# Kernel tuning notes

Hardware: AMD Instinct MI355X
Metric: run time of the kernel (lower is better)

Reference implementation:

```python
import jax, jax.numpy as jnp
from jax import lax
import numpy as np

B, T, F, H, L = 64, 2048, 8, 128, 2


def _uniform(key, shape, k):
    return jax.random.uniform(key, shape, jnp.float32, -k, k)


def setup_inputs() -> dict:
    key = jax.random.key(0)
    keys = jax.random.split(key, 12)
    k = 1.0 / np.sqrt(H)
    inp = {"x": jax.random.normal(keys[0], (B, T, F), jnp.float32)}
    # layer 0: input size F; layer 1: input size H (PyTorch nn.LSTM layout: gates i,f,g,o)
    inp["w_ih0"] = _uniform(keys[1], (4 * H, F), k)
    inp["w_hh0"] = _uniform(keys[2], (4 * H, H), k)
    inp["b_ih0"] = _uniform(keys[3], (4 * H,), k)
    inp["b_hh0"] = _uniform(keys[4], (4 * H,), k)
    inp["w_ih1"] = _uniform(keys[5], (4 * H, H), k)
    inp["w_hh1"] = _uniform(keys[6], (4 * H, H), k)
    inp["b_ih1"] = _uniform(keys[7], (4 * H,), k)
    inp["b_hh1"] = _uniform(keys[8], (4 * H,), k)
    inp["w_lin"] = _uniform(keys[9], (F, H), 1.0 / np.sqrt(H))
    inp["b_lin"] = _uniform(keys[10], (F,), 1.0 / np.sqrt(H))
    return inp


def _lstm_layer(x, w_ih, w_hh, b_ih, b_hh):
    # x: [B, T, D_in]; precompute input contribution to gates: [B, T, 4H]
    xg = jnp.einsum('btd,gd->btg', x, w_ih) + b_ih + b_hh
    h0 = jnp.zeros((x.shape[0], w_hh.shape[1]), x.dtype)
    c0 = jnp.zeros_like(h0)

    def step(carry, xg_t):
        h, c = carry
        gates = xg_t + h @ w_hh.T  # [B, 4H]
        i, f, g, o = jnp.split(gates, 4, axis=-1)
        i = jax.nn.sigmoid(i)
        f = jax.nn.sigmoid(f)
        g = jnp.tanh(g)
        o = jax.nn.sigmoid(o)
        c = f * c + i * g
        h = o * jnp.tanh(c)
        return (h, c), h

    _, hs = lax.scan(step, (h0, c0), jnp.swapaxes(xg, 0, 1))  # hs: [T, B, H]
    return jnp.swapaxes(hs, 0, 1)


def reference(x, w_ih0, w_hh0, b_ih0, b_hh0, w_ih1, w_hh1, b_ih1, b_hh1, w_lin, b_lin):
    h = _lstm_layer(x, w_ih0, w_hh0, b_ih0, b_hh0)
    h = _lstm_layer(h, w_ih1, w_hh1, b_ih1, b_hh1)
    return jnp.einsum('bth,fh->btf', h, w_lin) + b_lin
```

## Files before the change

kernel.cpp:

```cpp
#include <hip/hip_runtime.h>

#define B_ 64
#define T_ 2048
#define F_ 8
#define H_ 128
#define RING_LD 68
#define CHUNK 64
#define NCH (T_ / CHUNK)
#define GRING 16
#define H0_DW (CHUNK * 64)

typedef _Float16 v2h   __attribute__((ext_vector_type(2)));
typedef _Float16 f16x8 __attribute__((ext_vector_type(8)));
typedef float    f32x4 __attribute__((ext_vector_type(4)));

__device__ __forceinline__ unsigned pk2h(float lo, float hi) {
    v2h p;
    p[0] = (_Float16)lo;
    p[1] = (_Float16)hi;
    return __builtin_bit_cast(unsigned, p);
}

#if __has_builtin(__builtin_amdgcn_fdot2)
__device__ __forceinline__ float fdot2a(unsigned a, unsigned b, float c) {
    return __builtin_amdgcn_fdot2(__builtin_bit_cast(v2h, a),
                                  __builtin_bit_cast(v2h, b), c, false);
}
#else
__device__ __forceinline__ float fdot2a(unsigned a, unsigned b, float c) {
    v2h av = __builtin_bit_cast(v2h, a);
    v2h bv = __builtin_bit_cast(v2h, b);
    c += (float)av[0] * (float)bv[0];
    c += (float)av[1] * (float)bv[1];
    return c;
}
#endif

__device__ __forceinline__ float sigm(float x) {
    return 1.0f / (1.0f + __expf(-x));
}
__device__ __forceinline__ float tanh_f(float x) {
    float e = __expf(2.0f * x);
    return 1.0f - 2.0f / (e + 1.0f);
}

__device__ __forceinline__ f32x4 mfma16(f16x8 a, f16x8 b, f32x4 c) {
    return __builtin_amdgcn_mfma_f32_16x16x32_f16(a, b, c, 0, 0, 0);
}

#if __has_builtin(__builtin_amdgcn_mov_dpp)
template <int CTRL>
__device__ __forceinline__ float qperm(float v) {
    int i = __builtin_bit_cast(int, v);
    i = __builtin_amdgcn_mov_dpp(i, CTRL, 0xF, 0xF, true);
    return __builtin_bit_cast(float, i);
}
__device__ __forceinline__ float lane_xor1(float v) { return qperm<0xB1>(v); }
__device__ __forceinline__ float lane_xor2(float v) { return qperm<0x4E>(v); }
#else
__device__ __forceinline__ float lane_xor1(float v) {
    int i = __builtin_amdgcn_ds_swizzle(__builtin_bit_cast(int, v), 0x041F);
    return __builtin_bit_cast(float, i);
}
__device__ __forceinline__ float lane_xor2(float v) {
    int i = __builtin_amdgcn_ds_swizzle(__builtin_bit_cast(int, v), 0x081F);
    return __builtin_bit_cast(float, i);
}
#endif

__global__ __launch_bounds__(512, 2)
void lstm2_pc_kernel(const float* __restrict__ x,
                     const float* __restrict__ wih0,
                     const float* __restrict__ whh0,
                     const float* __restrict__ bih0,
                     const float* __restrict__ bhh0,
                     const float* __restrict__ wih1,
                     const float* __restrict__ whh1,
                     const float* __restrict__ bih1,
                     const float* __restrict__ bhh1,
                     const float* __restrict__ wlin,
                     const float* __restrict__ blin,
                     unsigned* __restrict__ h0g,
                     int* __restrict__ flags,
                     float* __restrict__ out)
{
    __shared__ __align__(16) unsigned arena[12288];
    __shared__ float blin_f[F_];

    const int tid = threadIdx.x;
    int* prog = flags;
    int* done = flags + 64;

    if (blockIdx.x < 64) {
        const int b = blockIdx.x;
        unsigned* x_lds = arena;
        unsigned* ring  = arena + 8192;

        const int h_idx = tid >> 2;
        const int sub   = tid & 3;
        const int growA = (0x3120 >> (sub * 4)) & 0xF;
        const int rowA  = growA * H_ + h_idx;

        const float4* xp = (const float4*)(x + (size_t)b * T_ * F_);
        #pragma unroll
        for (int i = 0; i < 8; ++i) {
            int idx = tid + i * 512;
            float4 v = xp[idx];
            x_lds[idx * 2 + 0] = pk2h(v.x, v.y);
            x_lds[idx * 2 + 1] = pk2h(v.z, v.w);
        }

        unsigned rwih0[4];
        {
            const float4* p = (const float4*)(wih0 + (size_t)rowA * F_);
            float4 v0 = p[0], v1 = p[1];
            rwih0[0] = pk2h(v0.x, v0.y); rwih0[1] = pk2h(v0.z, v0.w);
            rwih0[2] = pk2h(v1.x, v1.y); rwih0[3] = pk2h(v1.z, v1.w);
        }
        unsigned rwhh0[64];
        {
            const float4* p = (const float4*)(whh0 + (size_t)rowA * H_);
            #pragma unroll
            for (int i = 0; i < 32; ++i) {
                float4 v = p[i];
                rwhh0[i * 2 + 0] = pk2h(v.x, v.y);
                rwhh0[i * 2 + 1] = pk2h(v.z, v.w);
            }
        }
        const float bias0 = bih0[rowA] + bhh0[rowA];

        if (tid < 64) ring[63 * 64 + tid] = 0u;
        __syncthreads();

        const bool is_g = (sub == 1);
        const bool lo2  = (sub < 2);
        float c0 = 0.0f;

        for (int t = 0; t < T_; ++t) {
            {
                float aa = bias0, ab = 0.0f;
                uint4 xv = *(const uint4*)&x_lds[t * 4];
                aa = fdot2a(rwih0[0], xv.x, aa);
                ab = fdot2a(rwih0[1], xv.y, ab);
                aa = fdot2a(rwih0[2], xv.z, aa);
                ab = fdot2a(rwih0[3], xv.w, ab);
                const unsigned* hr = &ring[((t + 63) & 63) * 64];
                #pragma unroll
                for (int j = 0; j < 16; ++j) {
                    uint4 hv = *(const uint4*)&hr[j * 4];
                    aa = fdot2a(rwhh0[j * 4 + 0], hv.x, aa);
                    ab = fdot2a(rwhh0[j * 4 + 1], hv.y, ab);
                    aa = fdot2a(rwhh0[j * 4 + 2], hv.z, aa);
                    ab = fdot2a(rwhh0[j * 4 + 3], hv.w, ab);
                }
                float a = aa + ab;
                float xin = is_g ? 2.0f * a : a;
                float s   = sigm(xin);
                float act = is_g ? 2.0f * s - 1.0f : s;
                float s1  = lane_xor1(act);
                float p   = lo2 ? act * s1 : (sub == 2 ? act : s1) * c0;
                float cn  = p + lane_xor2(p);
                c0 = cn;
                float oval = (sub == 2) ? s1 : act;
                float h = oval * tanh_f(cn);
                if (sub == 2) ((_Float16*)&ring[(t & 63) * 64])[h_idx] = (_Float16)h;
            }
            __syncthreads();

            if ((t & 63) == 63) {
                const int c = t >> 6;
                if (c >= GRING) {
                    while (__hip_atomic_load(&done[b], __ATOMIC_ACQUIRE,
                                             __HIP_MEMORY_SCOPE_AGENT) < c - GRING + 1)
                        __builtin_amdgcn_s_sleep(8);
                    __syncthreads();
                }
                unsigned* dst = h0g + ((size_t)b * GRING + (c & (GRING - 1))) * H0_DW;
                uint4 v0 = *(const uint4*)&ring[tid * 8];
                uint4 v1 = *(const uint4*)&ring[tid * 8 + 4];
                *(uint4*)&dst[tid * 8]     = v0;
                *(uint4*)&dst[tid * 8 + 4] = v1;
                __syncthreads();
                if (tid == 0)
                    __hip_atomic_store(&prog[b], c + 1, __ATOMIC_RELEASE,
                                       __HIP_MEMORY_SCOPE_AGENT);
            }
        }
    } else {
        const int b = blockIdx.x - 64;
        unsigned* h0c    = arena;
        unsigned* h1ring = arena + 4096;
        unsigned* wlin_p = arena + 4096 + 64 * RING_LD;

        const int w   = tid >> 6;
        const int l   = tid & 63;
        const int n   = l & 15;
        const int grp = l >> 4;

        f16x8 wih1f[4][4], whh1f[4][4];
        #pragma unroll
        for (int j = 0; j < 4; ++j) {
            const int row = j * H_ + w * 16 + n;
            #pragma unroll
            for (int s = 0; s < 4; ++s) {
                const float* p1 = wih1 + (size_t)row * H_ + s * 32 + grp * 8;
                const float* p2 = whh1 + (size_t)row * H_ + s * 32 + grp * 8;
                f16x8 f1, f2;
                #pragma unroll
                for (int jj = 0; jj < 8; ++jj) {
                    f1[jj] = (_Float16)p1[jj];
                    f2[jj] = (_Float16)p2[jj];
                }
                wih1f[j][s] = f1;
                whh1f[j][s] = f2;
            }
        }
        #pragma unroll
        for (int j = 0; j < 4; ++j)
            #pragma unroll
            for (int s = 0; s < 4; ++s) {
                asm("" : "+a"(wih1f[j][s]));
                asm("" : "+a"(whh1f[j][s]));
            }

        float bb1[4];
        #pragma unroll
        for (int j = 0; j < 4; ++j) {
            const int row = j * H_ + w * 16 + n;
            bb1[j] = bih1[row] + bhh1[row];
        }
        {
            float2 v = ((const float2*)wlin)[tid];
            wlin_p[(tid >> 6) * RING_LD + (tid & 63)] = pk2h(v.x, v.y);
        }
        if (tid < F_) blin_f[tid] = blin[tid];
        if (tid < 64) h1ring[63 * RING_LD + tid] = 0u;
        __syncthreads();

        float c1 = 0.0f;
        const f32x4 Z4 = {0.0f, 0.0f, 0.0f, 0.0f};

        for (int c = 0; c < NCH; ++c) {
            while (__hip_atomic_load(&prog[b], __ATOMIC_ACQUIRE,
                                     __HIP_MEMORY_SCOPE_AGENT) < c + 1)
                __builtin_amdgcn_s_sleep(8);
            const unsigned* src = h0g + ((size_t)b * GRING + (c & (GRING - 1))) * H0_DW;
            uint4 v0 = *(const uint4*)&src[tid * 8];
            uint4 v1 = *(const uint4*)&src[tid * 8 + 4];
            *(uint4*)&h0c[tid * 8]     = v0;
            *(uint4*)&h0c[tid * 8 + 4] = v1;
            __syncthreads();
            if (tid == 0)
                __hip_atomic_store(&done[b], c + 1, __ATOMIC_RELAXED,
                                   __HIP_MEMORY_SCOPE_AGENT);

            for (int tk = 0; tk < CHUNK; ++tk) {
                const unsigned* h0r = &h0c[tk * 64];
                const unsigned* h1r = &h1ring[((tk + 63) & 63) * RING_LD];
                f32x4 acc[4];
                {
                    f16x8 ah = __builtin_bit_cast(f16x8, *(const uint4*)&h0r[grp * 4]);
                    #pragma unroll
                    for (int j = 0; j < 4; ++j) acc[j] = mfma16(ah, wih1f[j][0], Z4);
                }
                #pragma unroll
                for (int s = 1; s < 4; ++s) {
                    f16x8 ah = __builtin_bit_cast(f16x8,
                                   *(const uint4*)&h0r[s * 16 + grp * 4]);
                    #pragma unroll
                    for (int j = 0; j < 4; ++j) acc[j] = mfma16(ah, wih1f[j][s], acc[j]);
                }
                #pragma unroll
                for (int s = 0; s < 4; ++s) {
                    f16x8 ah = __builtin_bit_cast(f16x8,
                                   *(const uint4*)&h1r[s * 16 + grp * 4]);
                    #pragma unroll
                    for (int j = 0; j < 4; ++j) acc[j] = mfma16(ah, whh1f[j][s], acc[j]);
                }
                float gi = sigm(acc[0][0] + bb1[0]);
                float gf = sigm(acc[1][0] + bb1[1]);
                float gg = tanh_f(acc[2][0] + bb1[2]);
                float go = sigm(acc[3][0] + bb1[3]);
                c1 = gf * c1 + gi * gg;
                float hh = go * tanh_f(c1);
                if (l < 16)
                    ((_Float16*)&h1ring[tk * RING_LD])[w * 16 + l] = (_Float16)hh;
                __syncthreads();
            }

            {
                const int tick_i = tid >> 3;
                const int fo     = tid & 7;
                const unsigned* hp = &h1ring[tick_i * RING_LD];
                const unsigned* wv = &wlin_p[fo * RING_LD];
                float a = 0.0f;
                #pragma unroll
                for (int j = 0; j < 16; ++j) {
                    uint4 hv = *(const uint4*)&hp[j * 4];
                    uint4 wq = *(const uint4*)&wv[j * 4];
                    a = fdot2a(wq.x, hv.x, a);
                    a = fdot2a(wq.y, hv.y, a);
                    a = fdot2a(wq.z, hv.z, a);
                    a = fdot2a(wq.w, hv.w, a);
                }
                out[(size_t)b * T_ * F_ + (size_t)c * CHUNK * F_ + tid] = a + blin_f[fo];
            }
        }
    }
}

__global__ __launch_bounds__(512, 2)
void lstm2_burst_kernel(const float* __restrict__ x,
                        const float* __restrict__ wih0,
                        const float* __restrict__ whh0,
                        const float* __restrict__ bih0,
                        const float* __restrict__ bhh0,
                        const float* __restrict__ wih1,
                        const float* __restrict__ whh1,
                        const float* __restrict__ bih1,
                        const float* __restrict__ bhh1,
                        const float* __restrict__ wlin,
                        const float* __restrict__ blin,
                        float* __restrict__ out)
{
    __shared__ __align__(16) unsigned x_lds[T_ * F_ / 2];
    __shared__ __align__(16) unsigned h0_p[2][H_ / 2];
    __shared__ __align__(16) unsigned h1_ring[64 * RING_LD];
    __shared__ __align__(16) unsigned wlin_p[F_ * RING_LD];
    __shared__ float blin_f[F_];

    const int tid   = threadIdx.x;
    const int b     = blockIdx.x;
    const int h_idx = tid >> 2;
    const int sub   = tid & 3;
    const int grow  = (0x3120 >> (sub * 4)) & 0xF;
    const int row   = grow * H_ + h_idx;

    const float4* xp = (const float4*)(x + (size_t)b * T_ * F_);
    #pragma unroll
    for (int i = 0; i < 8; ++i) {
        int idx = tid + i * 512;
        float4 v = xp[idx];
        x_lds[idx * 2 + 0] = pk2h(v.x, v.y);
        x_lds[idx * 2 + 1] = pk2h(v.z, v.w);
    }

    unsigned rwih0[4];
    {
        const float4* p = (const float4*)(wih0 + (size_t)row * F_);
        float4 v0 = p[0], v1 = p[1];
        rwih0[0] = pk2h(v0.x, v0.y); rwih0[1] = pk2h(v0.z, v0.w);
        rwih0[2] = pk2h(v1.x, v1.y); rwih0[3] = pk2h(v1.z, v1.w);
    }
    unsigned rwhh0[64], rwih1[64], rwhh1[64];
    {
        const float4* p = (const float4*)(whh0 + (size_t)row * H_);
        #pragma unroll
        for (int i = 0; i < 32; ++i) {
            float4 v = p[i];
            rwhh0[i * 2 + 0] = pk2h(v.x, v.y);
            rwhh0[i * 2 + 1] = pk2h(v.z, v.w);
        }
    }
    {
        const float4* p = (const float4*)(wih1 + (size_t)row * H_);
        #pragma unroll
        for (int i = 0; i < 32; ++i) {
            float4 v = p[i];
            rwih1[i * 2 + 0] = pk2h(v.x, v.y);
            rwih1[i * 2 + 1] = pk2h(v.z, v.w);
        }
    }
    {
        const float4* p = (const float4*)(whh1 + (size_t)row * H_);
        #pragma unroll
        for (int i = 0; i < 32; ++i) {
            float4 v = p[i];
            rwhh1[i * 2 + 0] = pk2h(v.x, v.y);
            rwhh1[i * 2 + 1] = pk2h(v.z, v.w);
        }
    }
    const float bias0 = bih0[row] + bhh0[row];
    const float bias1 = bih1[row] + bhh1[row];

    {
        int r = tid >> 6, c = tid & 63;
        float2 v = ((const float2*)wlin)[r * 64 + c];
        wlin_p[r * RING_LD + c] = pk2h(v.x, v.y);
    }
    if (tid < F_) blin_f[tid] = blin[tid];
    if (tid < H_ / 2) { h0_p[0][tid] = 0u; h0_p[1][tid] = 0u; }
    if (tid < H_ / 2) h1_ring[63 * RING_LD + tid] = 0u;
    __syncthreads();

    const bool is_g = (sub == 1);
    const bool lo2  = (sub < 2);
    float c0 = 0.0f, c1 = 0.0f;

    for (int t = 0; t < T_; ++t) {
        const int rp = (t + 1) & 1;
        const int wp = t & 1;
        {
            float aa = bias0, ab = 0.0f;
            uint4 xv = *(const uint4*)&x_lds[t * 4];
            aa = fdot2a(rwih0[0], xv.x, aa);
            ab = fdot2a(rwih0[1], xv.y, ab);
            aa = fdot2a(rwih0[2], xv.z, aa);
            ab = fdot2a(rwih0[3], xv.w, ab);
            const unsigned* hr = &h0_p[rp][0];
            #pragma unroll
            for (int j = 0; j < 16; ++j) {
                uint4 hv = *(const uint4*)&hr[j * 4];
                aa = fdot2a(rwhh0[j * 4 + 0], hv.x, aa);
                ab = fdot2a(rwhh0[j * 4 + 1], hv.y, ab);
                aa = fdot2a(rwhh0[j * 4 + 2], hv.z, aa);
                ab = fdot2a(rwhh0[j * 4 + 3], hv.w, ab);
            }
            float a = aa + ab;
            float xin = is_g ? 2.0f * a : a;
            float s   = sigm(xin);
            float act = is_g ? 2.0f * s - 1.0f : s;
            float s1  = lane_xor1(act);
            float p   = lo2 ? act * s1 : (sub == 2 ? act : s1) * c0;
            float cn  = p + lane_xor2(p);
            c0 = cn;
            float oval = (sub == 2) ? s1 : act;
            float h = oval * tanh_f(cn);
            if (sub == 2) ((_Float16*)&h0_p[wp][0])[h_idx] = (_Float16)h;
        }
        __syncthreads();
        {
            float aa = bias1, ab = 0.0f, ba = 0.0f, bb = 0.0f;
            const unsigned* h0r = &h0_p[wp][0];
            const unsigned* h1r = &h1_ring[((t + 63) & 63) * RING_LD];
            #pragma unroll
            for (int j = 0; j < 16; ++j) {
                uint4 hv0 = *(const uint4*)&h0r[j * 4];
                uint4 hv1 = *(const uint4*)&h1r[j * 4];
                aa = fdot2a(rwih1[j * 4 + 0], hv0.x, aa);
                ab = fdot2a(rwih1[j * 4 + 1], hv0.y, ab);
                aa = fdot2a(rwih1[j * 4 + 2], hv0.z, aa);
                ab = fdot2a(rwih1[j * 4 + 3], hv0.w, ab);
                ba = fdot2a(rwhh1[j * 4 + 0], hv1.x, ba);
                bb = fdot2a(rwhh1[j * 4 + 1], hv1.y, bb);
                ba = fdot2a(rwhh1[j * 4 + 2], hv1.z, ba);
                bb = fdot2a(rwhh1[j * 4 + 3], hv1.w, bb);
            }
            float a = (aa + ab) + (ba + bb);
            float xin = is_g ? 2.0f * a : a;
            float s   = sigm(xin);
            float act = is_g ? 2.0f * s - 1.0f : s;
            float s1  = lane_xor1(act);
            float p   = lo2 ? act * s1 : (sub == 2 ? act : s1) * c1;
            float cn  = p + lane_xor2(p);
            c1 = cn;
            float oval = (sub == 2) ? s1 : act;
            float h = oval * tanh_f(cn);
            if (sub == 2)
                ((_Float16*)&h1_ring[(t & 63) * RING_LD])[h_idx] = (_Float16)h;
        }
        __syncthreads();
        if ((t & 63) == 63) {
            const int tick_i = tid >> 3;
            const int fo     = tid & 7;
            const unsigned* hp = &h1_ring[tick_i * RING_LD];
            const unsigned* wv = &wlin_p[fo * RING_LD];
            float a = 0.0f;
            #pragma unroll
            for (int j = 0; j < 16; ++j) {
                uint4 hv = *(const uint4*)&hp[j * 4];
                uint4 wq = *(const uint4*)&wv[j * 4];
                a = fdot2a(wq.x, hv.x, a);
                a = fdot2a(wq.y, hv.y, a);
                a = fdot2a(wq.z, hv.z, a);
                a = fdot2a(wq.w, hv.w, a);
            }
            out[(size_t)b * T_ * F_ + (size_t)(t - 63) * F_ + tid] = a + blin_f[fo];
        }
    }
}

extern "C" void kernel_launch(void* const* d_in, const int* in_sizes, int n_in,
                              void* d_out, int out_size, void* d_ws, size_t ws_size,
                              hipStream_t stream) {
    const float* x    = (const float*)d_in[0];
    const float* wih0 = (const float*)d_in[1];
    const float* whh0 = (const float*)d_in[2];
    const float* bih0 = (const float*)d_in[3];
    const float* bhh0 = (const float*)d_in[4];
    const float* wih1 = (const float*)d_in[5];
    const float* whh1 = (const float*)d_in[6];
    const float* bih1 = (const float*)d_in[7];
    const float* bhh1 = (const float*)d_in[8];
    const float* wlin = (const float*)d_in[9];
    const float* blin = (const float*)d_in[10];
    float* out = (float*)d_out;

    const size_t h0_bytes = (size_t)B_ * GRING * H0_DW * sizeof(unsigned);
    const size_t need = h0_bytes + 512;
    if (d_ws != nullptr && ws_size >= need) {
        unsigned* h0g = (unsigned*)d_ws;
        int* flags = (int*)((char*)d_ws + h0_bytes);
        hipMemsetAsync(flags, 0, 512, stream);
        lstm2_pc_kernel<<<dim3(128), dim3(512), 0, stream>>>(
            x, wih0, whh0, bih0, bhh0, wih1, whh1, bih1, bhh1, wlin, blin,
            h0g, flags, out);
    } else {
        lstm2_burst_kernel<<<dim3(B_), dim3(512), 0, stream>>>(
            x, wih0, whh0, bih0, bhh0, wih1, whh1, bih1, bhh1, wlin, blin, out);
    }
}
```

Measured before the change: 1.808 ms.

## Batch layer-1 input projection per half-chunk and split layer-0 dot-product chains

In the layer-1 consumer blocks, the input-to-hidden projection is taken out of the per-timestep recurrence. It is now computed as batched MFMA tiles over 16 time rows at a time and stored in a new LDS buffer, so each serial step only runs the hidden-to-hidden MFMAs and adds the precomputed values. The layer-0 producer splits its fdot2 accumulation into four independent chains instead of two, which shortens the serial dependency latency on each timestep. The LDS arena roughly doubles and the h0 chunk gets a padded stride; the larger footprint may limit blocks per CU.

```diff
diff --git a/kernel.cpp b/kernel.cpp
--- a/kernel.cpp
+++ b/kernel.cpp
@@ -9,6 +9,8 @@
 #define NCH (T_ / CHUNK)
 #define GRING 16
 #define H0_DW (CHUNK * 64)
+#define H0C_LD 68
+#define Z_LD 516
 
 typedef _Float16 v2h   __attribute__((ext_vector_type(2)));
 typedef _Float16 f16x8 __attribute__((ext_vector_type(8)));
@@ -69,22 +71,22 @@
 #endif
 
 __global__ __launch_bounds__(512, 2)
-void lstm2_pc_kernel(const float* __restrict__ x,
-                     const float* __restrict__ wih0,
-                     const float* __restrict__ whh0,
-                     const float* __restrict__ bih0,
-                     const float* __restrict__ bhh0,
-                     const float* __restrict__ wih1,
-                     const float* __restrict__ whh1,
-                     const float* __restrict__ bih1,
-                     const float* __restrict__ bhh1,
-                     const float* __restrict__ wlin,
-                     const float* __restrict__ blin,
-                     unsigned* __restrict__ h0g,
-                     int* __restrict__ flags,
-                     float* __restrict__ out)
+void lstm2_pc3_kernel(const float* __restrict__ x,
+                      const float* __restrict__ wih0,
+                      const float* __restrict__ whh0,
+                      const float* __restrict__ bih0,
+                      const float* __restrict__ bhh0,
+                      const float* __restrict__ wih1,
+                      const float* __restrict__ whh1,
+                      const float* __restrict__ bih1,
+                      const float* __restrict__ bhh1,
+                      const float* __restrict__ wlin,
+                      const float* __restrict__ blin,
+                      unsigned* __restrict__ h0g,
+                      int* __restrict__ flags,
+                      float* __restrict__ out)
 {
-    __shared__ __align__(16) unsigned arena[12288];
+    __shared__ __align__(16) unsigned arena[25760];
     __shared__ float blin_f[F_];
 
     const int tid = threadIdx.x;
@@ -138,22 +140,22 @@
 
         for (int t = 0; t < T_; ++t) {
             {
-                float aa = bias0, ab = 0.0f;
+                float aa = bias0, ab = 0.0f, ba = 0.0f, bb = 0.0f;
                 uint4 xv = *(const uint4*)&x_lds[t * 4];
                 aa = fdot2a(rwih0[0], xv.x, aa);
                 ab = fdot2a(rwih0[1], xv.y, ab);
-                aa = fdot2a(rwih0[2], xv.z, aa);
-                ab = fdot2a(rwih0[3], xv.w, ab);
+                ba = fdot2a(rwih0[2], xv.z, ba);
+                bb = fdot2a(rwih0[3], xv.w, bb);
                 const unsigned* hr = &ring[((t + 63) & 63) * 64];
                 #pragma unroll
                 for (int j = 0; j < 16; ++j) {
                     uint4 hv = *(const uint4*)&hr[j * 4];
                     aa = fdot2a(rwhh0[j * 4 + 0], hv.x, aa);
                     ab = fdot2a(rwhh0[j * 4 + 1], hv.y, ab);
-                    aa = fdot2a(rwhh0[j * 4 + 2], hv.z, aa);
-                    ab = fdot2a(rwhh0[j * 4 + 3], hv.w, ab);
+                    ba = fdot2a(rwhh0[j * 4 + 2], hv.z, ba);
+                    bb = fdot2a(rwhh0[j * 4 + 3], hv.w, bb);
                 }
-                float a = aa + ab;
+                float a = (aa + ab) + (ba + bb);
                 float xin = is_g ? 2.0f * a : a;
                 float s   = sigm(xin);
                 float act = is_g ? 2.0f * s - 1.0f : s;
@@ -189,8 +191,9 @@
     } else {
         const int b = blockIdx.x - 64;
         unsigned* h0c    = arena;
-        unsigned* h1ring = arena + 4096;
-        unsigned* wlin_p = arena + 4096 + 64 * RING_LD;
+        unsigned* h1ring = arena + 4352;
+        float*    zih1   = (float*)(arena + 8704);
+        unsigned* wlin_p = arena + 25216;
 
         const int w   = tid >> 6;
         const int l   = tid & 63;
@@ -245,47 +248,76 @@
                                      __HIP_MEMORY_SCOPE_AGENT) < c + 1)
                 __builtin_amdgcn_s_sleep(8);
             const unsigned* src = h0g + ((size_t)b * GRING + (c & (GRING - 1))) * H0_DW;
-            uint4 v0 = *(const uint4*)&src[tid * 8];
-            uint4 v1 = *(const uint4*)&src[tid * 8 + 4];
-            *(uint4*)&h0c[tid * 8]     = v0;
-            *(uint4*)&h0c[tid * 8 + 4] = v1;
+            {
+                const int tick = tid >> 3;
+                const int off  = (tid & 7) * 8;
+                uint4 v0 = *(const uint4*)&src[tick * 64 + off];
+                uint4 v1 = *(const uint4*)&src[tick * 64 + off + 4];
+                *(uint4*)&h0c[tick * H0C_LD + off]     = v0;
+                *(uint4*)&h0c[tick * H0C_LD + off + 4] = v1;
+            }
             __syncthreads();
             if (tid == 0)
                 __hip_atomic_store(&done[b], c + 1, __ATOMIC_RELAXED,
                                    __HIP_MEMORY_SCOPE_AGENT);
 
-            for (int tk = 0; tk < CHUNK; ++tk) {
-                const unsigned* h0r = &h0c[tk * 64];
-                const unsigned* h1r = &h1ring[((tk + 63) & 63) * RING_LD];
-                f32x4 acc[4];
-                {
-                    f16x8 ah = __builtin_bit_cast(f16x8, *(const uint4*)&h0r[grp * 4]);
+            for (int half = 0; half < 2; ++half) {
+                #pragma unroll
+                for (int mt = 0; mt < 2; ++mt) {
+                    f32x4 d0 = Z4, d1 = Z4, d2 = Z4, d3 = Z4;
+                    const int trow = half * 32 + mt * 16 + n;
                     #pragma unroll
-                    for (int j = 0; j < 4; ++j) acc[j] = mfma16(ah, wih1f[j][0], Z4);
+                    for (int s = 0; s < 4; ++s) {
+                        f16x8 ah = __builtin_bit_cast(
+                            f16x8, *(const uint4*)&h0c[trow * H0C_LD + s * 16 + grp * 4]);
+                        d0 = mfma16(ah, wih1f[0][s], d0);
+                        d1 = mfma16(ah, wih1f[1][s], d1);
+                        d2 = mfma16(ah, wih1f[2][s], d2);
+                        d3 = mfma16(ah, wih1f[3][s], d3);
+                    }
+                    const int zr = mt * 16 + grp * 4;
+                    #pragma unroll
+                    for (int reg = 0; reg < 4; ++reg) {
+                        zih1[(zr + reg) * Z_LD + 0 * H_ + w * 16 + n] = d0[reg];
+                        zih1[(zr + reg) * Z_LD + 1 * H_ + w * 16 + n] = d1[reg];
+                        zih1[(zr + reg) * Z_LD + 2 * H_ + w * 16 + n] = d2[reg];
+                        zih1[(zr + reg) * Z_LD + 3 * H_ + w * 16 + n] = d3[reg];
+                    }
                 }
-                #pragma unroll
-                for (int s = 1; s < 4; ++s) {
-                    f16x8 ah = __builtin_bit_cast(f16x8,
-                                   *(const uint4*)&h0r[s * 16 + grp * 4]);
+
+                for (int tk = 0; tk < 32; ++tk) {
+                    const int t  = c * CHUNK + half * 32 + tk;
+                    const unsigned* h1r = &h1ring[((t + 63) & 63) * RING_LD];
+                    f32x4 a0, a1, a2, a3;
+                    {
+                        f16x8 ah = __builtin_bit_cast(f16x8, *(const uint4*)&h1r[grp * 4]);
+                        a0 = mfma16(ah, whh1f[0][0], Z4);
+                        a1 = mfma16(ah, whh1f[1][0], Z4);
+                        a2 = mfma16(ah, whh1f[2][0], Z4);
+                        a3 = mfma16(ah, whh1f[3][0], Z4);
+                    }
                     #pragma unroll
-                    for (int j = 0; j < 4; ++j) acc[j] = mfma16(ah, wih1f[j][s], acc[j]);
+                    for (int s = 1; s < 4; ++s) {
+                        f16x8 ah = __builtin_bit_cast(
+                            f16x8, *(const uint4*)&h1r[s * 16 + grp * 4]);
+                        a0 = mfma16(ah, whh1f[0][s], a0);
+                        a1 = mfma16(ah, whh1f[1][s], a1);
+                        a2 = mfma16(ah, whh1f[2][s], a2);
+                        a3 = mfma16(ah, whh1f[3][s], a3);
+                    }
+                    const int zbase = (half * 32 + tk) * 0 + tk;
+                    const float* zp = &zih1[(half * 32 + tk - half * 32) * Z_LD];
+                    float gi = sigm(a0[0] + zp[0 * H_ + w * 16 + n] + bb1[0]);
+                    float gf = sigm(a1[0] + zp[1 * H_ + w * 16 + n] + bb1[1]);
+                    float gg = tanh_f(a2[0] + zp[2 * H_ + w * 16 + n] + bb1[2]);
+                    float go = sigm(a3[0] + zp[3 * H_ + w * 16 + n] + bb1[3]);
+                    (void)zbase;
+                    c1 = gf * c1 + gi * gg;
+                    float hh = go * tanh_f(c1);
+                    if (l < 16)
+                        ((_Float16*)&h1ring[(t & 63) * RING_LD])[w * 16 + l] = (_Float16)hh;
+                    __syncthreads();
                 }
-                #pragma unroll
-                for (int s = 0; s < 4; ++s) {
-                    f16x8 ah = __builtin_bit_cast(f16x8,
-                                   *(const uint4*)&h1r[s * 16 + grp * 4]);
-                    #pragma unroll
-                    for (int j = 0; j < 4; ++j) acc[j] = mfma16(ah, whh1f[j][s], acc[j]);
-                }
-                float gi = sigm(acc[0][0] + bb1[0]);
-                float gf = sigm(acc[1][0] + bb1[1]);
-                float gg = tanh_f(acc[2][0] + bb1[2]);
-                float go = sigm(acc[3][0] + bb1[3]);
-                c1 = gf * c1 + gi * gg;
-                float hh = go * tanh_f(c1);
-                if (l < 16)
-                    ((_Float16*)&h1ring[tk * RING_LD])[w * 16 + l] = (_Float16)hh;
-                __syncthreads();
             }
 
             {
@@ -502,7 +534,7 @@
         unsigned* h0g = (unsigned*)d_ws;
         int* flags = (int*)((char*)d_ws + h0_bytes);
         hipMemsetAsync(flags, 0, 512, stream);
-        lstm2_pc_kernel<<<dim3(128), dim3(512), 0, stream>>>(
+        lstm2_pc3_kernel<<<dim3(128), dim3(512), 0, stream>>>(
             x, wih0, whh0, bih0, bhh0, wih1, whh1, bih1, bhh1, wlin, blin,
             h0g, flags, out);
     } else {
```

Result: faster. 1.495 ms (-17.3%).

## Process two batch rows per block and batch layer-1 input projection via MFMA

Applied to the files above, without the earlier changes.

Each producer and consumer block now handles two batch sequences instead of one, halving the grid to 64 blocks and interleaving two independent recurrences for more instruction-level parallelism. The layer-1 input-gate projection is computed in 16-step tiles with MFMA directly from global h0 into an LDS z buffer, rather than per step from an LDS copy. The done flag now signals after the chunk finishes. This trades fewer active CUs and larger LDS use for better latency hiding within the serial recurrence.

```diff
diff --git a/kernel.cpp b/kernel.cpp
--- a/kernel.cpp
+++ b/kernel.cpp
@@ -9,6 +9,7 @@
 #define NCH (T_ / CHUNK)
 #define GRING 16
 #define H0_DW (CHUNK * 64)
+#define Z_LD 516
 
 typedef _Float16 v2h   __attribute__((ext_vector_type(2)));
 typedef _Float16 f16x8 __attribute__((ext_vector_type(8)));
@@ -69,45 +70,54 @@
 #endif
 
 __global__ __launch_bounds__(512, 2)
-void lstm2_pc_kernel(const float* __restrict__ x,
-                     const float* __restrict__ wih0,
-                     const float* __restrict__ whh0,
-                     const float* __restrict__ bih0,
-                     const float* __restrict__ bhh0,
-                     const float* __restrict__ wih1,
-                     const float* __restrict__ whh1,
-                     const float* __restrict__ bih1,
-                     const float* __restrict__ bhh1,
-                     const float* __restrict__ wlin,
-                     const float* __restrict__ blin,
-                     unsigned* __restrict__ h0g,
-                     int* __restrict__ flags,
-                     float* __restrict__ out)
+void lstm2_pc4_kernel(const float* __restrict__ x,
+                      const float* __restrict__ wih0,
+                      const float* __restrict__ whh0,
+                      const float* __restrict__ bih0,
+                      const float* __restrict__ bhh0,
+                      const float* __restrict__ wih1,
+                      const float* __restrict__ whh1,
+                      const float* __restrict__ bih1,
+                      const float* __restrict__ bhh1,
+                      const float* __restrict__ wlin,
+                      const float* __restrict__ blin,
+                      unsigned* __restrict__ h0g,
+                      int* __restrict__ flags,
+                      float* __restrict__ out)
 {
-    __shared__ __align__(16) unsigned arena[12288];
+    __shared__ __align__(16) unsigned arena[25760];
     __shared__ float blin_f[F_];
 
     const int tid = threadIdx.x;
     int* prog = flags;
     int* done = flags + 64;
 
-    if (blockIdx.x < 64) {
-        const int b = blockIdx.x;
-        unsigned* x_lds = arena;
-        unsigned* ring  = arena + 8192;
+    if (blockIdx.x < 32) {
+        const int b0 = blockIdx.x * 2;
+        const int b1 = b0 + 1;
+        unsigned* x0 = arena;
+        unsigned* x1 = arena + 8192;
+        unsigned* r0 = arena + 16384;
+        unsigned* r1 = arena + 20480;
 
         const int h_idx = tid >> 2;
         const int sub   = tid & 3;
         const int growA = (0x3120 >> (sub * 4)) & 0xF;
         const int rowA  = growA * H_ + h_idx;
 
-        const float4* xp = (const float4*)(x + (size_t)b * T_ * F_);
-        #pragma unroll
-        for (int i = 0; i < 8; ++i) {
-            int idx = tid + i * 512;
-            float4 v = xp[idx];
-            x_lds[idx * 2 + 0] = pk2h(v.x, v.y);
-            x_lds[idx * 2 + 1] = pk2h(v.z, v.w);
+        {
+            const float4* xp0 = (const float4*)(x + (size_t)b0 * T_ * F_);
+            const float4* xp1 = (const float4*)(x + (size_t)b1 * T_ * F_);
+            #pragma unroll
+            for (int i = 0; i < 8; ++i) {
+                int idx = tid + i * 512;
+                float4 v0 = xp0[idx];
+                float4 v1 = xp1[idx];
+                x0[idx * 2 + 0] = pk2h(v0.x, v0.y);
+                x0[idx * 2 + 1] = pk2h(v0.z, v0.w);
+                x1[idx * 2 + 0] = pk2h(v1.x, v1.y);
+                x1[idx * 2 + 1] = pk2h(v1.z, v1.w);
+            }
         }
 
         unsigned rwih0[4];
@@ -129,68 +139,107 @@
         }
         const float bias0 = bih0[rowA] + bhh0[rowA];
 
-        if (tid < 64) ring[63 * 64 + tid] = 0u;
+        if (tid < 64) { r0[63 * 64 + tid] = 0u; r1[63 * 64 + tid] = 0u; }
         __syncthreads();
 
         const bool is_g = (sub == 1);
         const bool lo2  = (sub < 2);
-        float c0 = 0.0f;
+        float c0_0 = 0.0f, c0_1 = 0.0f;
 
         for (int t = 0; t < T_; ++t) {
             {
-                float aa = bias0, ab = 0.0f;
-                uint4 xv = *(const uint4*)&x_lds[t * 4];
-                aa = fdot2a(rwih0[0], xv.x, aa);
-                ab = fdot2a(rwih0[1], xv.y, ab);
-                aa = fdot2a(rwih0[2], xv.z, aa);
-                ab = fdot2a(rwih0[3], xv.w, ab);
-                const unsigned* hr = &ring[((t + 63) & 63) * 64];
+                float aa0 = bias0, ab0 = 0.0f, ba0 = 0.0f, bb0 = 0.0f;
+                float aa1 = bias0, ab1 = 0.0f, ba1 = 0.0f, bb1 = 0.0f;
+                uint4 xv0 = *(const uint4*)&x0[t * 4];
+                uint4 xv1 = *(const uint4*)&x1[t * 4];
+                aa0 = fdot2a(rwih0[0], xv0.x, aa0);
+                ab0 = fdot2a(rwih0[1], xv0.y, ab0);
+                ba0 = fdot2a(rwih0[2], xv0.z, ba0);
+                bb0 = fdot2a(rwih0[3], xv0.w, bb0);
+                aa1 = fdot2a(rwih0[0], xv1.x, aa1);
+                ab1 = fdot2a(rwih0[1], xv1.y, ab1);
+                ba1 = fdot2a(rwih0[2], xv1.z, ba1);
+                bb1 = fdot2a(rwih0[3], xv1.w, bb1);
+                const unsigned* h0r = &r0[((t + 63) & 63) * 64];
+                const unsigned* h1r = &r1[((t + 63) & 63) * 64];
                 #pragma unroll
                 for (int j = 0; j < 16; ++j) {
-                    uint4 hv = *(const uint4*)&hr[j * 4];
-                    aa = fdot2a(rwhh0[j * 4 + 0], hv.x, aa);
-                    ab = fdot2a(rwhh0[j * 4 + 1], hv.y, ab);
-                    aa = fdot2a(rwhh0[j * 4 + 2], hv.z, aa);
-                    ab = fdot2a(rwhh0[j * 4 + 3], hv.w, ab);
-                }
-                float a = aa + ab;
-                float xin = is_g ? 2.0f * a : a;
-                float s   = sigm(xin);
-                float act = is_g ? 2.0f * s - 1.0f : s;
-                float s1  = lane_xor1(act);
-                float p   = lo2 ? act * s1 : (sub == 2 ? act : s1) * c0;
-                float cn  = p + lane_xor2(p);
-                c0 = cn;
-                float oval = (sub == 2) ? s1 : act;
-                float h = oval * tanh_f(cn);
-                if (sub == 2) ((_Float16*)&ring[(t & 63) * 64])[h_idx] = (_Float16)h;
+                    uint4 hv0 = *(const uint4*)&h0r[j * 4];
+                    uint4 hv1 = *(const uint4*)&h1r[j * 4];
+                    aa0 = fdot2a(rwhh0[j * 4 + 0], hv0.x, aa0);
+                    ab0 = fdot2a(rwhh0[j * 4 + 1], hv0.y, ab0);
+                    ba0 = fdot2a(rwhh0[j * 4 + 2], hv0.z, ba0);
+                    bb0 = fdot2a(rwhh0[j * 4 + 3], hv0.w, bb0);
+                    aa1 = fdot2a(rwhh0[j * 4 + 0], hv1.x, aa1);
+                    ab1 = fdot2a(rwhh0[j * 4 + 1], hv1.y, ab1);
+                    ba1 = fdot2a(rwhh0[j * 4 + 2], hv1.z, ba1);
+                    bb1 = fdot2a(rwhh0[j * 4 + 3], hv1.w, bb1);
+                }
+                float a0 = (aa0 + ab0) + (ba0 + bb0);
+                float a1 = (aa1 + ab1) + (ba1 + bb1);
+                float xin0 = is_g ? 2.0f * a0 : a0;
+                float xin1 = is_g ? 2.0f * a1 : a1;
+                float s0 = sigm(xin0);
+                float s1v = sigm(xin1);
+                float act0 = is_g ? 2.0f * s0 - 1.0f : s0;
+                float act1 = is_g ? 2.0f * s1v - 1.0f : s1v;
+                float sx0 = lane_xor1(act0);
+                float sx1 = lane_xor1(act1);
+                float p0 = lo2 ? act0 * sx0 : (sub == 2 ? act0 : sx0) * c0_0;
+                float p1 = lo2 ? act1 * sx1 : (sub == 2 ? act1 : sx1) * c0_1;
+                float cn0 = p0 + lane_xor2(p0);
+                float cn1 = p1 + lane_xor2(p1);
+                c0_0 = cn0;
+                c0_1 = cn1;
+                float ov0 = (sub == 2) ? sx0 : act0;
+                float ov1 = (sub == 2) ? sx1 : act1;
+                float hh0 = ov0 * tanh_f(cn0);
+                float hh1 = ov1 * tanh_f(cn1);
+                if (sub == 2) {
+                    ((_Float16*)&r0[(t & 63) * 64])[h_idx] = (_Float16)hh0;
+                    ((_Float16*)&r1[(t & 63) * 64])[h_idx] = (_Float16)hh1;
+                }
             }
             __syncthreads();
 
             if ((t & 63) == 63) {
                 const int c = t >> 6;
                 if (c >= GRING) {
-                    while (__hip_atomic_load(&done[b], __ATOMIC_ACQUIRE,
+                    while (__hip_atomic_load(&done[b0], __ATOMIC_ACQUIRE,
+                                             __HIP_MEMORY_SCOPE_AGENT) < c - GRING + 1 ||
+                           __hip_atomic_load(&done[b1], __ATOMIC_ACQUIRE,
                                              __HIP_MEMORY_SCOPE_AGENT) < c - GRING + 1)
                         __builtin_amdgcn_s_sleep(8);
                     __syncthreads();
                 }
-                unsigned* dst = h0g + ((size_t)b * GRING + (c & (GRING - 1))) * H0_DW;
-                uint4 v0 = *(const uint4*)&ring[tid * 8];
-                uint4 v1 = *(const uint4*)&ring[tid * 8 + 4];
-                *(uint4*)&dst[tid * 8]     = v0;
-                *(uint4*)&dst[tid * 8 + 4] = v1;
+                unsigned* d0 = h0g + ((size_t)b0 * GRING + (c & (GRING - 1))) * H0_DW;
+                unsigned* d1 = h0g + ((size_t)b1 * GRING + (c & (GRING - 1))) * H0_DW;
+                uint4 u0 = *(const uint4*)&r0[tid * 8];
+                uint4 u1 = *(const uint4*)&r0[tid * 8 + 4];
+                uint4 u2 = *(const uint4*)&r1[tid * 8];
+                uint4 u3 = *(const uint4*)&r1[tid * 8 + 4];
+                *(uint4*)&d0[tid * 8]     = u0;
+                *(uint4*)&d0[tid * 8 + 4] = u1;
+                *(uint4*)&d1[tid * 8]     = u2;
+                *(uint4*)&d1[tid * 8 + 4] = u3;
                 __syncthreads();
-                if (tid == 0)
-                    __hip_atomic_store(&prog[b], c + 1, __ATOMIC_RELEASE,
+                if (tid == 0) {
+                    __hip_atomic_store(&prog[b0], c + 1, __ATOMIC_RELEASE,
                                        __HIP_MEMORY_SCOPE_AGENT);
+                    __hip_atomic_store(&prog[b1], c + 1, __ATOMIC_RELEASE,
+                                       __HIP_MEMORY_SCOPE_AGENT);
+                }
             }
         }
     } else {
-        const int b = blockIdx.x - 64;
-        unsigned* h0c    = arena;
-        unsigned* h1ring = arena + 4096;
-        unsigned* wlin_p = arena + 4096 + 64 * RING_LD;
+        const int cb = blockIdx.x - 32;
+        const int b0 = cb * 2;
+        const int b1 = b0 + 1;
+        unsigned* ring0  = arena;
+        unsigned* ring1  = arena + 4352;
+        float*    z0     = (float*)(arena + 8704);
+        float*    z1     = (float*)(arena + 16960);
+        unsigned* wlin_p = arena + 25216;
 
         const int w   = tid >> 6;
         const int l   = tid & 63;
@@ -234,76 +283,143 @@
             wlin_p[(tid >> 6) * RING_LD + (tid & 63)] = pk2h(v.x, v.y);
         }
         if (tid < F_) blin_f[tid] = blin[tid];
-        if (tid < 64) h1ring[63 * RING_LD + tid] = 0u;
+        if (tid < 64) {
+            ring0[63 * RING_LD + tid] = 0u;
+            ring1[63 * RING_LD + tid] = 0u;
+        }
         __syncthreads();
 
-        float c1 = 0.0f;
+        float c1_0 = 0.0f, c1_1 = 0.0f;
         const f32x4 Z4 = {0.0f, 0.0f, 0.0f, 0.0f};
 
         for (int c = 0; c < NCH; ++c) {
-            while (__hip_atomic_load(&prog[b], __ATOMIC_ACQUIRE,
+            while (__hip_atomic_load(&prog[b0], __ATOMIC_ACQUIRE,
+                                     __HIP_MEMORY_SCOPE_AGENT) < c + 1 ||
+                   __hip_atomic_load(&prog[b1], __ATOMIC_ACQUIRE,
                                      __HIP_MEMORY_SCOPE_AGENT) < c + 1)
                 __builtin_amdgcn_s_sleep(8);
-            const unsigned* src = h0g + ((size_t)b * GRING + (c & (GRING - 1))) * H0_DW;
-            uint4 v0 = *(const uint4*)&src[tid * 8];
-            uint4 v1 = *(const uint4*)&src[tid * 8 + 4];
-            *(uint4*)&h0c[tid * 8]     = v0;
-            *(uint4*)&h0c[tid * 8 + 4] = v1;
-            __syncthreads();
-            if (tid == 0)
-                __hip_atomic_store(&done[b], c + 1, __ATOMIC_RELAXED,
-                                   __HIP_MEMORY_SCOPE_AGENT);
+            const unsigned* src0 = h0g + ((size_t)b0 * GRING + (c & (GRING - 1))) * H0_DW;
+            const unsigned* src1 = h0g + ((size_t)b1 * GRING + (c & (GRING - 1))) * H0_DW;
 
             for (int tk = 0; tk < CHUNK; ++tk) {
-                const unsigned* h0r = &h0c[tk * 64];
-                const unsigned* h1r = &h1ring[((tk + 63) & 63) * RING_LD];
-                f32x4 acc[4];
+                if ((tk & 15) == 0) {
+                    const int q = tk >> 4;
+                    const unsigned* a0p = src0 + (q * 16 + n) * 64;
+                    const unsigned* a1p = src1 + (q * 16 + n) * 64;
+                    f32x4 d0 = Z4, d1 = Z4, d2 = Z4, d3 = Z4;
+                    f32x4 e0 = Z4, e1 = Z4, e2 = Z4, e3 = Z4;
+                    #pragma unroll
+                    for (int s = 0; s < 4; ++s) {
+                        f16x8 ah0 = __builtin_bit_cast(
+                            f16x8, *(const uint4*)&a0p[s * 16 + grp * 4]);
+                        f16x8 ah1 = __builtin_bit_cast(
+                            f16x8, *(const uint4*)&a1p[s * 16 + grp * 4]);
+                        d0 = mfma16(ah0, wih1f[0][s], d0);
+                        d1 = mfma16(ah0, wih1f[1][s], d1);
+                        d2 = mfma16(ah0, wih1f[2][s], d2);
+                        d3 = mfma16(ah0, wih1f[3][s], d3);
+                        e0 = mfma16(ah1, wih1f[0][s], e0);
+                        e1 = mfma16(ah1, wih1f[1][s], e1);
+                        e2 = mfma16(ah1, wih1f[2][s], e2);
+                        e3 = mfma16(ah1, wih1f[3][s], e3);
+                    }
+                    #pragma unroll
+                    for (int reg = 0; reg < 4; ++reg) {
+                        const int zr = (grp * 4 + reg) * Z_LD + w * 16 + n;
+                        z0[zr + 0 * H_] = d0[reg];
+                        z0[zr + 1 * H_] = d1[reg];
+                        z0[zr + 2 * H_] = d2[reg];
+                        z0[zr + 3 * H_] = d3[reg];
+                        z1[zr + 0 * H_] = e0[reg];
+                        z1[zr + 1 * H_] = e1[reg];
+                        z1[zr + 2 * H_] = e2[reg];
+                        z1[zr + 3 * H_] = e3[reg];
+                    }
+                }
+
+                const int t = c * CHUNK + tk;
+                const unsigned* h1r0 = &ring0[((t + 63) & 63) * RING_LD];
+                const unsigned* h1r1 = &ring1[((t + 63) & 63) * RING_LD];
+                f32x4 a0, a1, a2, a3, g0, g1, g2, g3;
                 {
-                    f16x8 ah = __builtin_bit_cast(f16x8, *(const uint4*)&h0r[grp * 4]);
-                    #pragma unroll
-                    for (int j = 0; j < 4; ++j) acc[j] = mfma16(ah, wih1f[j][0], Z4);
+                    f16x8 ah0 = __builtin_bit_cast(f16x8, *(const uint4*)&h1r0[grp * 4]);
+                    f16x8 ah1 = __builtin_bit_cast(f16x8, *(const uint4*)&h1r1[grp * 4]);
+                    a0 = mfma16(ah0, whh1f[0][0], Z4);
+                    a1 = mfma16(ah0, whh1f[1][0], Z4);
+                    a2 = mfma16(ah0, whh1f[2][0], Z4);
+                    a3 = mfma16(ah0, whh1f[3][0], Z4);
+                    g0 = mfma16(ah1, whh1f[0][0], Z4);
+                    g1 = mfma16(ah1, whh1f[1][0], Z4);
+                    g2 = mfma16(ah1, whh1f[2][0], Z4);
+                    g3 = mfma16(ah1, whh1f[3][0], Z4);
                 }
                 #pragma unroll
                 for (int s = 1; s < 4; ++s) {
-                    f16x8 ah = __builtin_bit_cast(f16x8,
-                                   *(const uint4*)&h0r[s * 16 + grp * 4]);
+                    f16x8 ah0 = __builtin_bit_cast(
+                        f16x8, *(const uint4*)&h1r0[s * 16 + grp * 4]);
+                    f16x8 ah1 = __builtin_bit_cast(
+                        f16x8, *(const uint4*)&h1r1[s * 16 + grp * 4]);
+                    a0 = mfma16(ah0, whh1f[0][s], a0);
+                    a1 = mfma16(ah0, whh1f[1][s], a1);
+                    a2 = mfma16(ah0, whh1f[2][s], a2);
+                    a3 = mfma16(ah0, whh1f[3][s], a3);
+                    g0 = mfma16(ah1, whh1f[0][s], g0);
+                    g1 = mfma16(ah1, whh1f[1][s], g1);
+                    g2 = mfma16(ah1, whh1f[2][s], g2);
+                    g3 = mfma16(ah1, whh1f[3][s], g3);
+                }
+                const float* zp0 = &z0[(tk & 15) * Z_LD + w * 16 + n];
+                const float* zp1 = &z1[(tk & 15) * Z_LD + w * 16 + n];
+                float gi0 = sigm(a0[0] + zp0[0 * H_] + bb1[0]);
+                float gf0 = sigm(a1[0] + zp0[1 * H_] + bb1[1]);
+                float gg0 = tanh_f(a2[0] + zp0[2 * H_] + bb1[2]);
+                float go0 = sigm(a3[0] + zp0[3 * H_] + bb1[3]);
+                float gi1 = sigm(g0[0] + zp1[0 * H_] + bb1[0]);
+                float gf1 = sigm(g1[0] + zp1[1 * H_] + bb1[1]);
+                float gg1 = tanh_f(g2[0] + zp1[2 * H_] + bb1[2]);
+                float go1 = sigm(g3[0] + zp1[3 * H_] + bb1[3]);
+                c1_0 = gf0 * c1_0 + gi0 * gg0;
+                c1_1 = gf1 * c1_1 + gi1 * gg1;
+                float hh0 = go0 * tanh_f(c1_0);
+                float hh1 = go1 * tanh_f(c1_1);
+                if (l < 16) {
+                    ((_Float16*)&ring0[(t & 63) * RING_LD])[w * 16 + l] = (_Float16)hh0;
+                    ((_Float16*)&ring1[(t & 63) * RING_LD])[w * 16 + l] = (_Float16)hh1;
+                }
+                __syncthreads();
+            }
+
+            {
+                const int half = tid >> 8;
+                const unsigned* ringX = half ? ring1 : ring0;
+                const int bX = half ? b1 : b0;
+                #pragma unroll
+                for (int r = 0; r < 2; ++r) {
+                    const int idx    = (tid & 255) + r * 256;
+                    const int tick_i = idx >> 3;
+                    const int fo     = idx & 7;
+                    const unsigned* hp = &ringX[tick_i * RING_LD];
+                    const unsigned* wv = &wlin_p[fo * RING_LD];
+                    float a = 0.0f;
                     #pragma unroll
-                    for (int j = 0; j < 4; ++j) acc[j] = mfma16(ah, wih1f[j][s], acc[j]);
-                }
-                #pragma unroll
-                for (int s = 0; s < 4; ++s) {
-                    f16x8 ah = __builtin_bit_cast(f16x8,
-                                   *(const uint4*)&h1r[s * 16 + grp * 4]);
-                    #pragma unroll
-                    for (int j = 0; j < 4; ++j) acc[j] = mfma16(ah, whh1f[j][s], acc[j]);
-                }
-                float gi = sigm(acc[0][0] + bb1[0]);
-                float gf = sigm(acc[1][0] + bb1[1]);
-                float gg = tanh_f(acc[2][0] + bb1[2]);
-                float go = sigm(acc[3][0] + bb1[3]);
-                c1 = gf * c1 + gi * gg;
-                float hh = go * tanh_f(c1);
-                if (l < 16)
-                    ((_Float16*)&h1ring[tk * RING_LD])[w * 16 + l] = (_Float16)hh;
-                __syncthreads();
-            }
-
-            {
-                const int tick_i = tid >> 3;
-                const int fo     = tid & 7;
-                const unsigned* hp = &h1ring[tick_i * RING_LD];
-                const unsigned* wv = &wlin_p[fo * RING_LD];
-                float a = 0.0f;
-                #pragma unroll
-                for (int j = 0; j < 16; ++j) {
-                    uint4 hv = *(const uint4*)&hp[j * 4];
-                    uint4 wq = *(const uint4*)&wv[j * 4];
-                    a = fdot2a(wq.x, hv.x, a);
-                    a = fdot2a(wq.y, hv.y, a);
-                    a = fdot2a(wq.z, hv.z, a);
-                    a = fdot2a(wq.w, hv.w, a);
-                }
-                out[(size_t)b * T_ * F_ + (size_t)c * CHUNK * F_ + tid] = a + blin_f[fo];
+                    for (int j = 0; j < 16; ++j) {
+                        uint4 hv = *(const uint4*)&hp[j * 4];
+                        uint4 wq = *(const uint4*)&wv[j * 4];
+                        a = fdot2a(wq.x, hv.x, a);
+                        a = fdot2a(wq.y, hv.y, a);
+                        a = fdot2a(wq.z, hv.z, a);
+                        a = fdot2a(wq.w, hv.w, a);
+                    }
+                    out[(size_t)bX * T_ * F_ + (size_t)c * CHUNK * F_ + idx] =
+                        a + blin_f[fo];
+                }
+            }
+            __syncthreads();
+            if (tid == 0) {
+                __hip_atomic_store(&done[b0], c + 1, __ATOMIC_RELAXED,
+                                   __HIP_MEMORY_SCOPE_AGENT);
+                __hip_atomic_store(&done[b1], c + 1, __ATOMIC_RELAXED,
+                                   __HIP_MEMORY_SCOPE_AGENT);
             }
         }
     }
@@ -502,7 +618,7 @@
         unsigned* h0g = (unsigned*)d_ws;
         int* flags = (int*)((char*)d_ws + h0_bytes);
         hipMemsetAsync(flags, 0, 512, stream);
-        lstm2_pc_kernel<<<dim3(128), dim3(512), 0, stream>>>(
+        lstm2_pc4_kernel<<<dim3(64), dim3(512), 0, stream>>>(
             x, wih0, whh0, bih0, bhh0, wih1, whh1, bih1, bhh1, wlin, blin,
             h0g, flags, out);
     } else {
```

New measurement: 3.251 ms. +79.8%, slower.
